# Optimization experiments

Measured on AMD Instinct MI355X. Metric: run time of the kernel, lower is better.

## Reference

```python
import jax, jax.numpy as jnp
import numpy as np

K = 16          # neighbors per node
EPS = 1e-5      # BatchNorm eps
BN_SCALE = 1.0 / np.sqrt(1.0 + EPS)  # eval BN with running mean=0, var=1


def _knn_idx(x, k):
    # x: [B, N, d] -> idx [B, N, k] of k nearest neighbors (self excluded)
    sq = jnp.sum(x * x, axis=-1)                               # [B, N]
    d2 = sq[:, :, None] + sq[:, None, :] - 2.0 * jnp.einsum('bnd,bmd->bnm', x, x)
    n = x.shape[1]
    d2 = jnp.where(jnp.eye(n, dtype=bool)[None], jnp.inf, d2)  # no self loops
    _, idx = jax.lax.top_k(-d2, k)
    return idx


def _edge_conv(x, idx, W, b, g, be):
    # PyG EdgeConv: max_j MLP([x_i, x_j - x_i]); MLP = Linear+BN(eval)+ReLU
    xj = jax.vmap(lambda xb, ib: xb[ib])(x, idx)               # [B, N, k, d]
    xi = x[:, :, None, :]
    m = jnp.concatenate([jnp.broadcast_to(xi, xj.shape), xj - xi], axis=-1)
    h = m @ W + b                                              # [B, N, k, out]
    h = g * (h * BN_SCALE) + be                                # eval BatchNorm
    h = jax.nn.relu(h)
    return jnp.max(h, axis=2)                                  # scatter-max over k


def setup_inputs() -> dict:
    key = jax.random.key(0)
    ks = jax.random.split(key, 16)
    B, N, D, C = 128, 256, 6, 12

    def w(k_, shape, fan_in):
        return (jax.random.normal(k_, shape, jnp.float32) / np.sqrt(fan_in)).astype(jnp.float32)

    inp = {
        'x':   jax.random.normal(ks[0], (B, N, D), jnp.float32),
        'W1':  w(ks[1], (2 * 6, 64), 12),   'b1': jnp.zeros((64,), jnp.float32),
        'g1':  jnp.ones((64,), jnp.float32), 'be1': jnp.zeros((64,), jnp.float32),
        'W2':  w(ks[2], (2 * 64, 128), 128), 'b2': jnp.zeros((128,), jnp.float32),
        'g2':  jnp.ones((128,), jnp.float32), 'be2': jnp.zeros((128,), jnp.float32),
        'W3':  w(ks[3], (2 * 128, 256), 256), 'b3': jnp.zeros((256,), jnp.float32),
        'g3':  jnp.ones((256,), jnp.float32), 'be3': jnp.zeros((256,), jnp.float32),
        'Wf1': w(ks[4], (256, 128), 256),    'bf1': jnp.zeros((128,), jnp.float32),
        'gf':  jnp.ones((128,), jnp.float32), 'bef': jnp.zeros((128,), jnp.float32),
        'Wf2': w(ks[5], (128, C), 128),      'bf2': jnp.zeros((C,), jnp.float32),
    }
    return inp


def reference(x, W1, b1, g1, be1, W2, b2, g2, be2, W3, b3, g3, be3,
              Wf1, bf1, gf, bef, Wf2, bf2):
    h = _edge_conv(x, _knn_idx(x, K), W1, b1, g1, be1)   # [B, N, 64]
    h = _edge_conv(h, _knn_idx(h, K), W2, b2, g2, be2)   # [B, N, 128]
    h = _edge_conv(h, _knn_idx(h, K), W3, b3, g3, be3)   # [B, N, 256]
    p = jnp.max(h, axis=1)                               # global_max_pool [B, 256]
    f = jax.nn.relu(gf * ((p @ Wf1 + bf1) * BN_SCALE) + bef)
    return f @ Wf2 + bf2                                 # [B, num_classes]
```

## Files before the change

kernel.cpp:

```cpp
#include <hip/hip_runtime.h>
#include <cstdint>
#include <cstddef>

#define KNN 16
#define NPTS 256
#define NBATCH 128

static constexpr float BN_SCALE_F = 0.9999950000374997f;

__device__ inline unsigned int f32_ord(float f) {
    unsigned int u = __float_as_uint(f);
    return (u & 0x80000000u) ? ~u : (u | 0x80000000u);
}

template<int D>
__global__ __launch_bounds__(256) void sq_kernel(const float* __restrict__ x,
                                                 float* __restrict__ sq) {
    const int t = blockIdx.x * 256 + threadIdx.x;
    const float* r = x + (size_t)t * D;
    float s = 0.f;
    #pragma unroll
    for (int d = 0; d < D; ++d) s = fmaf(r[d], r[d], s);
    sq[t] = s;
}

template<int D>
__global__ __launch_bounds__(256) void gram_kernel(const float* __restrict__ x,
                                                   const float* __restrict__ sq,
                                                   float* __restrict__ d2) {
    constexpr int KS = (D >= 16) ? 16 : D;
    const int t  = threadIdx.x;
    const int tx = t & 15, ty = t >> 4;
    const int b    = blockIdx.x >> 4;
    const int tile = blockIdx.x & 15;
    const int i0 = (tile & 3) * 64;
    const int j0 = (tile >> 2) * 64;
    const int base = b * NPTS;

    __shared__ float As[KS][68];
    __shared__ float Bs[KS][68];

    float acc[4][4] = {};
    for (int k0 = 0; k0 < D; k0 += KS) {
        if constexpr (D % 16 == 0) {
            const int r  = t >> 2;
            const int cq = (t & 3) * 4;
            const float4 va = *(const float4*)(x + (size_t)(base + i0 + r) * D + k0 + cq);
            const float4 vb = *(const float4*)(x + (size_t)(base + j0 + r) * D + k0 + cq);
            As[cq + 0][r] = va.x; As[cq + 1][r] = va.y;
            As[cq + 2][r] = va.z; As[cq + 3][r] = va.w;
            Bs[cq + 0][r] = vb.x; Bs[cq + 1][r] = vb.y;
            Bs[cq + 2][r] = vb.z; Bs[cq + 3][r] = vb.w;
        } else {
            for (int e = t; e < 64 * KS; e += 256) {
                const int r = e / KS, c = e % KS;
                As[c][r] = x[(size_t)(base + i0 + r) * D + k0 + c];
                Bs[c][r] = x[(size_t)(base + j0 + r) * D + k0 + c];
            }
        }
        __syncthreads();
        #pragma unroll
        for (int kk = 0; kk < KS; ++kk) {
            const float4 av = *(const float4*)&As[kk][ty * 4];
            const float4 bv = *(const float4*)&Bs[kk][tx * 4];
            const float am[4] = {av.x, av.y, av.z, av.w};
            const float bm[4] = {bv.x, bv.y, bv.z, bv.w};
            #pragma unroll
            for (int m = 0; m < 4; ++m)
                #pragma unroll
                for (int n = 0; n < 4; ++n)
                    acc[m][n] = fmaf(am[m], bm[n], acc[m][n]);
        }
        __syncthreads();
    }

    float sqi[4], sqj[4];
    #pragma unroll
    for (int m = 0; m < 4; ++m) {
        sqi[m] = sq[base + i0 + ty * 4 + m];
        sqj[m] = sq[base + j0 + tx * 4 + m];
    }
    #pragma unroll
    for (int m = 0; m < 4; ++m) {
        const int gi = i0 + ty * 4 + m;
        float v[4];
        #pragma unroll
        for (int n = 0; n < 4; ++n) {
            v[n] = (sqi[m] + sqj[n]) - 2.f * acc[m][n];
            if (gi == j0 + tx * 4 + n) v[n] = INFINITY;
        }
        float4* dst = (float4*)(d2 + ((size_t)b << 16) + (size_t)gi * NPTS + j0 + tx * 4);
        *dst = make_float4(v[0], v[1], v[2], v[3]);
    }
}

__global__ __launch_bounds__(256) void topk_kernel(const float* __restrict__ d2,
                                                   int* __restrict__ idx) {
    const int t = threadIdx.x;
    const int p = t >> 3;
    const int q = t & 7;
    const int ig = blockIdx.x * 32 + p;
    const float* row = d2 + (size_t)ig * NPTS;

    unsigned long long L[16];
    #pragma unroll
    for (int r = 0; r < 16; ++r) L[r] = ~0ull;

    const int jb = q * 32;
    #pragma unroll
    for (int jj = 0; jj < 32; jj += 4) {
        const float4 v4 = *(const float4*)(row + jb + jj);
        const float vv[4] = {v4.x, v4.y, v4.z, v4.w};
        #pragma unroll
        for (int e = 0; e < 4; ++e) {
            const unsigned long long key =
                ((unsigned long long)f32_ord(vv[e]) << 32) |
                (unsigned int)(jb + jj + e);
            #pragma unroll
            for (int r = 15; r >= 1; --r)
                L[r] = (key < L[r]) ? ((key < L[r - 1]) ? L[r - 1] : key) : L[r];
            L[0] = (key < L[0]) ? key : L[0];
        }
    }

    __shared__ unsigned long long K[256][17];
    #pragma unroll
    for (int r = 0; r < 16; ++r) K[t][r] = L[r];
    __syncthreads();

    if (t < 32) {
        const int pp  = t;
        const int igo = blockIdx.x * 32 + pp;
        int h[8];
        unsigned long long v[8];
        #pragma unroll
        for (int c = 0; c < 8; ++c) { h[c] = 0; v[c] = K[pp * 8 + c][0]; }
        int outj[16];
        #pragma unroll
        for (int r = 0; r < 16; ++r) {
            unsigned long long best = v[0];
            #pragma unroll
            for (int c = 1; c < 8; ++c) best = (v[c] < best) ? v[c] : best;
            outj[r] = (int)(unsigned int)(best & 0xffffffffull);
            #pragma unroll
            for (int c = 0; c < 8; ++c) {
                const bool hit = (v[c] == best);
                const int hn = h[c] + (hit ? 1 : 0);
                const unsigned long long nv = K[pp * 8 + c][hn & 15];
                v[c] = hit ? ((hn < 16) ? nv : ~0ull) : v[c];
                h[c] = hn;
            }
        }
        int4* op = (int4*)(idx + (size_t)igo * KNN);
        op[0] = make_int4(outj[0],  outj[1],  outj[2],  outj[3]);
        op[1] = make_int4(outj[4],  outj[5],  outj[6],  outj[7]);
        op[2] = make_int4(outj[8],  outj[9],  outj[10], outj[11]);
        op[3] = make_int4(outj[12], outj[13], outj[14], outj[15]);
    }
}

template<int D, int C, int BNW>
__global__ __launch_bounds__(256) void mlp_gemm_kernel(
        const float* __restrict__ x, const float* __restrict__ W,
        const float* __restrict__ bias, const float* __restrict__ g,
        const float* __restrict__ be,
        float* __restrict__ A, float* __restrict__ Bv) {
    constexpr int BM = 128;
    constexpr int KT = (D >= 16) ? 16 : D;
    const int t  = threadIdx.x;
    const int m0 = blockIdx.x * BM;
    const int n0 = blockIdx.y * BNW;
    const int tx = t & 15;
    const int ty = t >> 4;

    __shared__ float Xs[KT][BM + 4];
    __shared__ float Ws[KT][BNW + 4];

    float acc[8][8] = {};

    for (int k0 = 0; k0 < D; k0 += KT) {
        if constexpr (D % 16 == 0) {
            const int r  = t >> 1;
            const int cq = (t & 1) * 8;
            const float* src = x + (size_t)(m0 + r) * D + k0 + cq;
            const float4 v0 = *(const float4*)(src);
            const float4 v1 = *(const float4*)(src + 4);
            Xs[cq + 0][r] = v0.x; Xs[cq + 1][r] = v0.y;
            Xs[cq + 2][r] = v0.z; Xs[cq + 3][r] = v0.w;
            Xs[cq + 4][r] = v1.x; Xs[cq + 5][r] = v1.y;
            Xs[cq + 6][r] = v1.z; Xs[cq + 7][r] = v1.w;
        } else {
            for (int e = t; e < BM * KT; e += 256) {
                const int r = e / KT, c = e % KT;
                Xs[c][r] = x[(size_t)(m0 + r) * D + k0 + c];
            }
        }
        if constexpr (D % 16 == 0) {
            const int wk = t >> 4;
            const int nq = (t & 15) * 8;
            const int gn = n0 + nq;
            const int kr = k0 + wk;
            if (gn < C) {
                const float* pt = W + (size_t)kr * C + gn;
                const float* pb = W + (size_t)(D + kr) * C + gn;
                const float4 t0 = *(const float4*)(pt);
                const float4 t1 = *(const float4*)(pt + 4);
                const float4 b0 = *(const float4*)(pb);
                const float4 b1 = *(const float4*)(pb + 4);
                Ws[wk][nq + 0] = t0.x - b0.x; Ws[wk][nq + 1] = t0.y - b0.y;
                Ws[wk][nq + 2] = t0.z - b0.z; Ws[wk][nq + 3] = t0.w - b0.w;
                Ws[wk][nq + 4] = t1.x - b1.x; Ws[wk][nq + 5] = t1.y - b1.y;
                Ws[wk][nq + 6] = t1.z - b1.z; Ws[wk][nq + 7] = t1.w - b1.w;
            } else {
                const float* pb = W + (size_t)(D + kr) * C + (gn - C);
                const float4 b0 = *(const float4*)(pb);
                const float4 b1 = *(const float4*)(pb + 4);
                Ws[wk][nq + 0] = b0.x; Ws[wk][nq + 1] = b0.y;
                Ws[wk][nq + 2] = b0.z; Ws[wk][nq + 3] = b0.w;
                Ws[wk][nq + 4] = b1.x; Ws[wk][nq + 5] = b1.y;
                Ws[wk][nq + 6] = b1.z; Ws[wk][nq + 7] = b1.w;
            }
        } else {
            for (int e = t; e < KT * BNW; e += 256) {
                const int k = e >> 7, n = e & (BNW - 1);
                const int gn = n0 + n, kr = k0 + k;
                if (gn < C)
                    Ws[k][n] = W[(size_t)kr * C + gn] - W[(size_t)(D + kr) * C + gn];
                else
                    Ws[k][n] = W[(size_t)(D + kr) * C + (gn - C)];
            }
        }
        __syncthreads();

        #pragma unroll
        for (int kk = 0; kk < KT; ++kk) {
            float xm[8], wn[8];
            *(float4*)&xm[0] = *(const float4*)&Xs[kk][ty * 8];
            *(float4*)&xm[4] = *(const float4*)&Xs[kk][ty * 8 + 4];
            *(float4*)&wn[0] = *(const float4*)&Ws[kk][tx * 8];
            *(float4*)&wn[4] = *(const float4*)&Ws[kk][tx * 8 + 4];
            #pragma unroll
            for (int m = 0; m < 8; ++m)
                #pragma unroll
                for (int n = 0; n < 8; ++n)
                    acc[m][n] = fmaf(xm[m], wn[n], acc[m][n]);
        }
        __syncthreads();
    }

    const int gn = n0 + tx * 8;
    if (gn < C) {
        float fac[8];
        #pragma unroll
        for (int e = 0; e < 8; ++e) fac[e] = g[gn + e] * BN_SCALE_F;
        #pragma unroll
        for (int m = 0; m < 8; ++m) {
            float o[8];
            #pragma unroll
            for (int e = 0; e < 8; ++e) o[e] = fac[e] * acc[m][e];
            float* dst = A + (size_t)(m0 + ty * 8 + m) * C + gn;
            *(float4*)(dst)     = make_float4(o[0], o[1], o[2], o[3]);
            *(float4*)(dst + 4) = make_float4(o[4], o[5], o[6], o[7]);
        }
    } else {
        const int cb = gn - C;
        float fac[8], bb[8], bee[8];
        #pragma unroll
        for (int e = 0; e < 8; ++e) {
            fac[e] = g[cb + e] * BN_SCALE_F;
            bb[e]  = bias[cb + e];
            bee[e] = be[cb + e];
        }
        #pragma unroll
        for (int m = 0; m < 8; ++m) {
            float o[8];
            #pragma unroll
            for (int e = 0; e < 8; ++e)
                o[e] = fmaf(fac[e], acc[m][e] + bb[e], bee[e]);
            float* dst = Bv + (size_t)(m0 + ty * 8 + m) * C + cb;
            *(float4*)(dst)     = make_float4(o[0], o[1], o[2], o[3]);
            *(float4*)(dst + 4) = make_float4(o[4], o[5], o[6], o[7]);
        }
    }
}

template<int C>
__global__ __launch_bounds__(C) void combine_kernel(
        const float* A, const float* __restrict__ Bv,
        const int* __restrict__ idx, float* out) {
    const int bi = blockIdx.x;
    const int c  = threadIdx.x;
    __shared__ int nbr[KNN];
    if (c < KNN) nbr[c] = idx[(size_t)bi * KNN + c];
    __syncthreads();
    const int b0 = bi & ~255;
    float mx = -INFINITY;
    #pragma unroll
    for (int kk = 0; kk < KNN; ++kk)
        mx = fmaxf(mx, Bv[(size_t)(b0 + nbr[kk]) * C + c]);
    float a = A[(size_t)bi * C + c];
    out[(size_t)bi * C + c] = fmaxf(a + mx, 0.f);
}

__global__ __launch_bounds__(256) void head_kernel(
        const float* __restrict__ h3, const float* __restrict__ Wf1,
        const float* __restrict__ bf1, const float* __restrict__ gf,
        const float* __restrict__ bef, const float* __restrict__ Wf2,
        const float* __restrict__ bf2, float* __restrict__ out) {
    const int b   = blockIdx.x;
    const int tid = threadIdx.x;
    __shared__ float p[256];
    __shared__ float f[128];
    const float* hb = h3 + (size_t)b * NPTS * 256;
    float mx = -INFINITY;
    for (int n = 0; n < NPTS; ++n) mx = fmaxf(mx, hb[(size_t)n * 256 + tid]);
    p[tid] = mx;
    __syncthreads();
    if (tid < 128) {
        float acc = bf1[tid];
        for (int d = 0; d < 256; ++d)
            acc = fmaf(p[d], Wf1[(size_t)d * 128 + tid], acc);
        float v = gf[tid] * (acc * BN_SCALE_F) + bef[tid];
        f[tid] = fmaxf(v, 0.f);
    }
    __syncthreads();
    if (tid < 12) {
        float acc = bf2[tid];
        for (int d = 0; d < 128; ++d)
            acc = fmaf(f[d], Wf2[(size_t)d * 12 + tid], acc);
        out[(size_t)b * 12 + tid] = acc;
    }
}

extern "C" void kernel_launch(void* const* d_in, const int* in_sizes, int n_in,
                              void* d_out, int out_size, void* d_ws, size_t ws_size,
                              hipStream_t stream) {
    const float* x   = (const float*)d_in[0];
    const float* W1  = (const float*)d_in[1];
    const float* b1  = (const float*)d_in[2];
    const float* g1  = (const float*)d_in[3];
    const float* be1 = (const float*)d_in[4];
    const float* W2  = (const float*)d_in[5];
    const float* b2  = (const float*)d_in[6];
    const float* g2  = (const float*)d_in[7];
    const float* be2 = (const float*)d_in[8];
    const float* W3  = (const float*)d_in[9];
    const float* b3  = (const float*)d_in[10];
    const float* g3  = (const float*)d_in[11];
    const float* be3 = (const float*)d_in[12];
    const float* Wf1 = (const float*)d_in[13];
    const float* bf1 = (const float*)d_in[14];
    const float* gf  = (const float*)d_in[15];
    const float* bef = (const float*)d_in[16];
    const float* Wf2 = (const float*)d_in[17];
    const float* bf2 = (const float*)d_in[18];
    float* out = (float*)d_out;

    char* ws = (char*)d_ws;
    const size_t idx_bytes = (size_t)NBATCH * NPTS * KNN * sizeof(int);
    const size_t reg_bytes = (size_t)NBATCH * NPTS * 256 * sizeof(float);
    int*   idx = (int*)ws;
    float* R1  = (float*)(ws + idx_bytes);
    float* R2  = (float*)(ws + idx_bytes + reg_bytes);
    float* R3  = (float*)(ws + idx_bytes + 2 * reg_bytes);
    float* sqb = (float*)(ws + idx_bytes + 3 * reg_bytes);

    const int BN = NBATCH * NPTS;
    const int GRAM_GRID = NBATCH * 16;
    const int TOPK_GRID = BN / 32;
    const int MB = BN / 128;

    sq_kernel<6><<<BN / 256, 256, 0, stream>>>(x, sqb);
    gram_kernel<6><<<GRAM_GRID, 256, 0, stream>>>(x, sqb, R3);
    topk_kernel<<<TOPK_GRID, 256, 0, stream>>>(R3, idx);
    mlp_gemm_kernel<6, 64, 128><<<dim3(MB, 1), 256, 0, stream>>>(
        x, W1, b1, g1, be1, R1, R2);
    combine_kernel<64><<<BN, 64, 0, stream>>>(R1, R2, idx, R1);

    sq_kernel<64><<<BN / 256, 256, 0, stream>>>(R1, sqb);
    gram_kernel<64><<<GRAM_GRID, 256, 0, stream>>>(R1, sqb, R3);
    topk_kernel<<<TOPK_GRID, 256, 0, stream>>>(R3, idx);
    mlp_gemm_kernel<64, 128, 128><<<dim3(MB, 2), 256, 0, stream>>>(
        R1, W2, b2, g2, be2, R2, R3);
    combine_kernel<128><<<BN, 128, 0, stream>>>(R2, R3, idx, R2);

    sq_kernel<128><<<BN / 256, 256, 0, stream>>>(R2, sqb);
    gram_kernel<128><<<GRAM_GRID, 256, 0, stream>>>(R2, sqb, R1);
    topk_kernel<<<TOPK_GRID, 256, 0, stream>>>(R1, idx);
    mlp_gemm_kernel<128, 256, 128><<<dim3(MB, 4), 256, 0, stream>>>(
        R2, W3, b3, g3, be3, R3, R1);
    combine_kernel<256><<<BN, 256, 0, stream>>>(R3, R1, idx, R3);

    head_kernel<<<NBATCH, 256, 0, stream>>>(R3, Wf1, bf1, gf, bef, Wf2, bf2, out);
}
```

Measured before the change: 486.5 us.

## Enlarge per-thread register tiles to 16x8 in gram and MLP GEMM kernels

Both the pairwise-distance gram kernel and the edge MLP GEMM now use 128-thread blocks, each thread computing a 16x8 output micro-tile. The gram kernel covers a 128x128 tile, cutting the grid from 16 to 4 blocks per batch. The A operand in shared memory gets a padded layout (stride 20 per 16 rows) to avoid bank conflicts on the wider reads. This raises FMA-to-shared-load ratio and data reuse, at the cost of more registers per thread, lower occupancy and fewer blocks in flight.

```diff
diff --git a/kernel.cpp b/kernel.cpp
--- a/kernel.cpp
+++ b/kernel.cpp
@@ -25,72 +25,85 @@
 }
 
 template<int D>
-__global__ __launch_bounds__(256) void gram_kernel(const float* __restrict__ x,
+__global__ __launch_bounds__(128) void gram_kernel(const float* __restrict__ x,
                                                    const float* __restrict__ sq,
                                                    float* __restrict__ d2) {
-    constexpr int KS = (D >= 16) ? 16 : D;
-    const int t  = threadIdx.x;
-    const int tx = t & 15, ty = t >> 4;
-    const int b    = blockIdx.x >> 4;
-    const int tile = blockIdx.x & 15;
-    const int i0 = (tile & 3) * 64;
-    const int j0 = (tile >> 2) * 64;
+    constexpr int KT = (D >= 16) ? 16 : D;
+    const int t = threadIdx.x;
+    const int w = t >> 6, l = t & 63;
+    const int tx8 = l & 7, ty8 = l >> 3;
+    const int rowL = ty8 * 16;
+    const int colL = w * 64 + tx8 * 8;
+    const int b    = blockIdx.x >> 2;
+    const int tile = blockIdx.x & 3;
+    const int i0 = (tile & 1) * 128;
+    const int j0 = (tile >> 1) * 128;
     const int base = b * NPTS;
 
-    __shared__ float As[KS][68];
-    __shared__ float Bs[KS][68];
-
-    float acc[4][4] = {};
-    for (int k0 = 0; k0 < D; k0 += KS) {
+    __shared__ float As[KT][160];
+    __shared__ float Bs[KT][132];
+
+    float acc[16][8] = {};
+    for (int k0 = 0; k0 < D; k0 += KT) {
         if constexpr (D % 16 == 0) {
-            const int r  = t >> 2;
-            const int cq = (t & 3) * 4;
-            const float4 va = *(const float4*)(x + (size_t)(base + i0 + r) * D + k0 + cq);
-            const float4 vb = *(const float4*)(x + (size_t)(base + j0 + r) * D + k0 + cq);
-            As[cq + 0][r] = va.x; As[cq + 1][r] = va.y;
-            As[cq + 2][r] = va.z; As[cq + 3][r] = va.w;
-            Bs[cq + 0][r] = vb.x; Bs[cq + 1][r] = vb.y;
-            Bs[cq + 2][r] = vb.z; Bs[cq + 3][r] = vb.w;
+            const float* pa = x + (size_t)(base + i0 + t) * D + k0;
+            const float* pb = x + (size_t)(base + j0 + t) * D + k0;
+            const int ca = t + 4 * (t >> 4);
+            #pragma unroll
+            for (int q = 0; q < 4; ++q) {
+                const float4 v = *(const float4*)(pa + q * 4);
+                As[q*4+0][ca] = v.x; As[q*4+1][ca] = v.y;
+                As[q*4+2][ca] = v.z; As[q*4+3][ca] = v.w;
+            }
+            #pragma unroll
+            for (int q = 0; q < 4; ++q) {
+                const float4 v = *(const float4*)(pb + q * 4);
+                Bs[q*4+0][t] = v.x; Bs[q*4+1][t] = v.y;
+                Bs[q*4+2][t] = v.z; Bs[q*4+3][t] = v.w;
+            }
         } else {
-            for (int e = t; e < 64 * KS; e += 256) {
-                const int r = e / KS, c = e % KS;
-                As[c][r] = x[(size_t)(base + i0 + r) * D + k0 + c];
-                Bs[c][r] = x[(size_t)(base + j0 + r) * D + k0 + c];
+            for (int e = t; e < 128 * KT; e += 128) {
+                const int r = e / KT, c = e % KT;
+                As[c][r + 4 * (r >> 4)] = x[(size_t)(base + i0 + r) * D + k0 + c];
+                Bs[c][r]                = x[(size_t)(base + j0 + r) * D + k0 + c];
             }
         }
         __syncthreads();
-        #pragma unroll
-        for (int kk = 0; kk < KS; ++kk) {
-            const float4 av = *(const float4*)&As[kk][ty * 4];
-            const float4 bv = *(const float4*)&Bs[kk][tx * 4];
-            const float am[4] = {av.x, av.y, av.z, av.w};
-            const float bm[4] = {bv.x, bv.y, bv.z, bv.w};
-            #pragma unroll
-            for (int m = 0; m < 4; ++m)
+        const int ra = ty8 * 20;
+        #pragma unroll
+        for (int kk = 0; kk < KT; ++kk) {
+            float am[16], bm[8];
+            *(float4*)&am[0]  = *(const float4*)&As[kk][ra];
+            *(float4*)&am[4]  = *(const float4*)&As[kk][ra + 4];
+            *(float4*)&am[8]  = *(const float4*)&As[kk][ra + 8];
+            *(float4*)&am[12] = *(const float4*)&As[kk][ra + 12];
+            *(float4*)&bm[0]  = *(const float4*)&Bs[kk][colL];
+            *(float4*)&bm[4]  = *(const float4*)&Bs[kk][colL + 4];
+            #pragma unroll
+            for (int m = 0; m < 16; ++m)
                 #pragma unroll
-                for (int n = 0; n < 4; ++n)
+                for (int n = 0; n < 8; ++n)
                     acc[m][n] = fmaf(am[m], bm[n], acc[m][n]);
         }
         __syncthreads();
     }
 
-    float sqi[4], sqj[4];
-    #pragma unroll
-    for (int m = 0; m < 4; ++m) {
-        sqi[m] = sq[base + i0 + ty * 4 + m];
-        sqj[m] = sq[base + j0 + tx * 4 + m];
-    }
-    #pragma unroll
-    for (int m = 0; m < 4; ++m) {
-        const int gi = i0 + ty * 4 + m;
-        float v[4];
-        #pragma unroll
-        for (int n = 0; n < 4; ++n) {
-            v[n] = (sqi[m] + sqj[n]) - 2.f * acc[m][n];
-            if (gi == j0 + tx * 4 + n) v[n] = INFINITY;
-        }
-        float4* dst = (float4*)(d2 + ((size_t)b << 16) + (size_t)gi * NPTS + j0 + tx * 4);
-        *dst = make_float4(v[0], v[1], v[2], v[3]);
+    float sqj[8];
+    #pragma unroll
+    for (int n = 0; n < 8; ++n) sqj[n] = sq[base + j0 + colL + n];
+    #pragma unroll
+    for (int m = 0; m < 16; ++m) {
+        const int gi = i0 + rowL + m;
+        const float sqi = sq[base + gi];
+        float v[8];
+        #pragma unroll
+        for (int n = 0; n < 8; ++n) {
+            v[n] = (sqi + sqj[n]) - 2.f * acc[m][n];
+            if (gi == j0 + colL + n) v[n] = INFINITY;
+        }
+        float* dst = d2 + ((size_t)b << 16) + (size_t)gi * NPTS + j0 + colL;
+        *(float4*)(dst)     = make_float4(v[0], v[1], v[2], v[3]);
+        *(float4*)(dst + 4) = make_float4(v[4], v[5], v[6], v[7]);
     }
 }
 
@@ -159,88 +172,83 @@
     }
 }
 
-template<int D, int C, int BNW>
-__global__ __launch_bounds__(256) void mlp_gemm_kernel(
+template<int D, int C>
+__global__ __launch_bounds__(128) void mlp_gemm_kernel(
         const float* __restrict__ x, const float* __restrict__ W,
         const float* __restrict__ bias, const float* __restrict__ g,
         const float* __restrict__ be,
         float* __restrict__ A, float* __restrict__ Bv) {
-    constexpr int BM = 128;
     constexpr int KT = (D >= 16) ? 16 : D;
-    const int t  = threadIdx.x;
-    const int m0 = blockIdx.x * BM;
-    const int n0 = blockIdx.y * BNW;
-    const int tx = t & 15;
-    const int ty = t >> 4;
-
-    __shared__ float Xs[KT][BM + 4];
-    __shared__ float Ws[KT][BNW + 4];
-
-    float acc[8][8] = {};
-
+    const int t = threadIdx.x;
+    const int w = t >> 6, l = t & 63;
+    const int tx8 = l & 7, ty8 = l >> 3;
+    const int colL = w * 64 + tx8 * 8;
+    const int m0 = blockIdx.x * 128;
+    const int n0 = blockIdx.y * 128;
+
+    __shared__ float Xs[KT][160];
+    __shared__ float Ws[KT][132];
+
+    float acc[16][8] = {};
     for (int k0 = 0; k0 < D; k0 += KT) {
         if constexpr (D % 16 == 0) {
-            const int r  = t >> 1;
-            const int cq = (t & 1) * 8;
-            const float* src = x + (size_t)(m0 + r) * D + k0 + cq;
-            const float4 v0 = *(const float4*)(src);
-            const float4 v1 = *(const float4*)(src + 4);
-            Xs[cq + 0][r] = v0.x; Xs[cq + 1][r] = v0.y;
-            Xs[cq + 2][r] = v0.z; Xs[cq + 3][r] = v0.w;
-            Xs[cq + 4][r] = v1.x; Xs[cq + 5][r] = v1.y;
-            Xs[cq + 6][r] = v1.z; Xs[cq + 7][r] = v1.w;
-        } else {
-            for (int e = t; e < BM * KT; e += 256) {
-                const int r = e / KT, c = e % KT;
-                Xs[c][r] = x[(size_t)(m0 + r) * D + k0 + c];
-            }
-        }
-        if constexpr (D % 16 == 0) {
-            const int wk = t >> 4;
-            const int nq = (t & 15) * 8;
-            const int gn = n0 + nq;
-            const int kr = k0 + wk;
+            const float* px = x + (size_t)(m0 + t) * D + k0;
+            const int ca = t + 4 * (t >> 4);
+            #pragma unroll
+            for (int q = 0; q < 4; ++q) {
+                const float4 v = *(const float4*)(px + q * 4);
+                Xs[q*4+0][ca] = v.x; Xs[q*4+1][ca] = v.y;
+                Xs[q*4+2][ca] = v.z; Xs[q*4+3][ca] = v.w;
+            }
+            const int wk = t & 15, nq = (t >> 4) * 16;
+            const int gn = n0 + nq, kr = k0 + wk;
             if (gn < C) {
                 const float* pt = W + (size_t)kr * C + gn;
                 const float* pb = W + (size_t)(D + kr) * C + gn;
-                const float4 t0 = *(const float4*)(pt);
-                const float4 t1 = *(const float4*)(pt + 4);
-                const float4 b0 = *(const float4*)(pb);
-                const float4 b1 = *(const float4*)(pb + 4);
-                Ws[wk][nq + 0] = t0.x - b0.x; Ws[wk][nq + 1] = t0.y - b0.y;
-                Ws[wk][nq + 2] = t0.z - b0.z; Ws[wk][nq + 3] = t0.w - b0.w;
-                Ws[wk][nq + 4] = t1.x - b1.x; Ws[wk][nq + 5] = t1.y - b1.y;
-                Ws[wk][nq + 6] = t1.z - b1.z; Ws[wk][nq + 7] = t1.w - b1.w;
+                #pragma unroll
+                for (int q = 0; q < 4; ++q) {
+                    const float4 a4 = *(const float4*)(pt + q * 4);
+                    const float4 b4 = *(const float4*)(pb + q * 4);
+                    Ws[wk][nq+q*4+0] = a4.x - b4.x;
+                    Ws[wk][nq+q*4+1] = a4.y - b4.y;
+                    Ws[wk][nq+q*4+2] = a4.z - b4.z;
+                    Ws[wk][nq+q*4+3] = a4.w - b4.w;
+                }
             } else {
                 const float* pb = W + (size_t)(D + kr) * C + (gn - C);
-                const float4 b0 = *(const float4*)(pb);
-                const float4 b1 = *(const float4*)(pb + 4);
-                Ws[wk][nq + 0] = b0.x; Ws[wk][nq + 1] = b0.y;
-                Ws[wk][nq + 2] = b0.z; Ws[wk][nq + 3] = b0.w;
-                Ws[wk][nq + 4] = b1.x; Ws[wk][nq + 5] = b1.y;
-                Ws[wk][nq + 6] = b1.z; Ws[wk][nq + 7] = b1.w;
+                #pragma unroll
+                for (int q = 0; q < 4; ++q) {
+                    const float4 b4 = *(const float4*)(pb + q * 4);
+                    Ws[wk][nq+q*4+0] = b4.x; Ws[wk][nq+q*4+1] = b4.y;
+                    Ws[wk][nq+q*4+2] = b4.z; Ws[wk][nq+q*4+3] = b4.w;
+                }
             }
         } else {
-            for (int e = t; e < KT * BNW; e += 256) {
-                const int k = e >> 7, n = e & (BNW - 1);
-                const int gn = n0 + n, kr = k0 + k;
-                if (gn < C)
-                    Ws[k][n] = W[(size_t)kr * C + gn] - W[(size_t)(D + kr) * C + gn];
-                else
-                    Ws[k][n] = W[(size_t)(D + kr) * C + (gn - C)];
+            for (int e = t; e < 128 * KT; e += 128) {
+                const int r = e / KT, c = e % KT;
+                Xs[c][r + 4 * (r >> 4)] = x[(size_t)(m0 + r) * D + k0 + c];
+            }
+            for (int e = t; e < KT * 128; e += 128) {
+                const int c = e >> 7, n = e & 127;
+                const int gn = n0 + n, kr = k0 + c;
+                Ws[c][n] = (gn < C)
+                    ? W[(size_t)kr * C + gn] - W[(size_t)(D + kr) * C + gn]
+                    : W[(size_t)(D + kr) * C + (gn - C)];
             }
         }
         __syncthreads();
-
+        const int ra = ty8 * 20;
         #pragma unroll
         for (int kk = 0; kk < KT; ++kk) {
-            float xm[8], wn[8];
-            *(float4*)&xm[0] = *(const float4*)&Xs[kk][ty * 8];
-            *(float4*)&xm[4] = *(const float4*)&Xs[kk][ty * 8 + 4];
-            *(float4*)&wn[0] = *(const float4*)&Ws[kk][tx * 8];
-            *(float4*)&wn[4] = *(const float4*)&Ws[kk][tx * 8 + 4];
-            #pragma unroll
-            for (int m = 0; m < 8; ++m)
+            float xm[16], wn[8];
+            *(float4*)&xm[0]  = *(const float4*)&Xs[kk][ra];
+            *(float4*)&xm[4]  = *(const float4*)&Xs[kk][ra + 4];
+            *(float4*)&xm[8]  = *(const float4*)&Xs[kk][ra + 8];
+            *(float4*)&xm[12] = *(const float4*)&Xs[kk][ra + 12];
+            *(float4*)&wn[0]  = *(const float4*)&Ws[kk][colL];
+            *(float4*)&wn[4]  = *(const float4*)&Ws[kk][colL + 4];
+            #pragma unroll
+            for (int m = 0; m < 16; ++m)
                 #pragma unroll
                 for (int n = 0; n < 8; ++n)
                     acc[m][n] = fmaf(xm[m], wn[n], acc[m][n]);
@@ -248,17 +256,17 @@
         __syncthreads();
     }
 
-    const int gn = n0 + tx * 8;
+    const int gn = n0 + colL;
     if (gn < C) {
         float fac[8];
         #pragma unroll
         for (int e = 0; e < 8; ++e) fac[e] = g[gn + e] * BN_SCALE_F;
         #pragma unroll
-        for (int m = 0; m < 8; ++m) {
+        for (int m = 0; m < 16; ++m) {
             float o[8];
             #pragma unroll
             for (int e = 0; e < 8; ++e) o[e] = fac[e] * acc[m][e];
-            float* dst = A + (size_t)(m0 + ty * 8 + m) * C + gn;
+            float* dst = A + (size_t)(m0 + ty8 * 16 + m) * C + gn;
             *(float4*)(dst)     = make_float4(o[0], o[1], o[2], o[3]);
             *(float4*)(dst + 4) = make_float4(o[4], o[5], o[6], o[7]);
         }
@@ -272,12 +280,12 @@
             bee[e] = be[cb + e];
         }
         #pragma unroll
-        for (int m = 0; m < 8; ++m) {
+        for (int m = 0; m < 16; ++m) {
             float o[8];
             #pragma unroll
             for (int e = 0; e < 8; ++e)
                 o[e] = fmaf(fac[e], acc[m][e] + bb[e], bee[e]);
-            float* dst = Bv + (size_t)(m0 + ty * 8 + m) * C + cb;
+            float* dst = Bv + (size_t)(m0 + ty8 * 16 + m) * C + cb;
             *(float4*)(dst)     = make_float4(o[0], o[1], o[2], o[3]);
             *(float4*)(dst + 4) = make_float4(o[4], o[5], o[6], o[7]);
         }
@@ -366,28 +374,28 @@
     float* sqb = (float*)(ws + idx_bytes + 3 * reg_bytes);
 
     const int BN = NBATCH * NPTS;
-    const int GRAM_GRID = NBATCH * 16;
+    const int GRAM_GRID = NBATCH * 4;
     const int TOPK_GRID = BN / 32;
     const int MB = BN / 128;
 
     sq_kernel<6><<<BN / 256, 256, 0, stream>>>(x, sqb);
-    gram_kernel<6><<<GRAM_GRID, 256, 0, stream>>>(x, sqb, R3);
+    gram_kernel<6><<<GRAM_GRID, 128, 0, stream>>>(x, sqb, R3);
     topk_kernel<<<TOPK_GRID, 256, 0, stream>>>(R3, idx);
-    mlp_gemm_kernel<6, 64, 128><<<dim3(MB, 1), 256, 0, stream>>>(
+    mlp_gemm_kernel<6, 64><<<dim3(MB, 1), 128, 0, stream>>>(
         x, W1, b1, g1, be1, R1, R2);
     combine_kernel<64><<<BN, 64, 0, stream>>>(R1, R2, idx, R1);
 
     sq_kernel<64><<<BN / 256, 256, 0, stream>>>(R1, sqb);
-    gram_kernel<64><<<GRAM_GRID, 256, 0, stream>>>(R1, sqb, R3);
+    gram_kernel<64><<<GRAM_GRID, 128, 0, stream>>>(R1, sqb, R3);
     topk_kernel<<<TOPK_GRID, 256, 0, stream>>>(R3, idx);
-    mlp_gemm_kernel<64, 128, 128><<<dim3(MB, 2), 256, 0, stream>>>(
+    mlp_gemm_kernel<64, 128><<<dim3(MB, 2), 128, 0, stream>>>(
         R1, W2, b2, g2, be2, R2, R3);
     combine_kernel<128><<<BN, 128, 0, stream>>>(R2, R3, idx, R2);
 
     sq_kernel<128><<<BN / 256, 256, 0, stream>>>(R2, sqb);
-    gram_kernel<128><<<GRAM_GRID, 256, 0, stream>>>(R2, sqb, R1);
+    gram_kernel<128><<<GRAM_GRID, 128, 0, stream>>>(R2, sqb, R1);
     topk_kernel<<<TOPK_GRID, 256, 0, stream>>>(R1, idx);
-    mlp_gemm_kernel<128, 256, 128><<<dim3(MB, 4), 256, 0, stream>>>(
+    mlp_gemm_kernel<128, 256><<<dim3(MB, 4), 128, 0, stream>>>(
         R2, W3, b3, g3, be3, R3, R1);
     combine_kernel<256><<<BN, 256, 0, stream>>>(R3, R1, idx, R3);
 
```

Result: slower. 516.2 us (+6.1%).
